# Performance work log

Hardware: AMD Instinct MI355X
Metric: run time of the kernel (lower is better)

Reference implementation:

```python
import jax, jax.numpy as jnp
import numpy as np

TAU = 2.0        # LIFNode tau
ALPHA = 4.0      # spikingjelly default Sigmoid surrogate alpha
SCALE = 0.125    # attention scale from SSA
EPS = 1e-5       # BatchNorm eps

@jax.custom_vjp
def heaviside(x):
    return (x >= 0).astype(x.dtype)

def _hv_fwd(x):
    return (x >= 0).astype(x.dtype), x

def _hv_bwd(x, g):
    s = jax.nn.sigmoid(ALPHA * x)
    return (g * ALPHA * s * (1.0 - s),)

heaviside.defvjp(_hv_fwd, _hv_bwd)

def lif(x_seq, v_th):
    """Multi-step LIF (decay_input=True, v_reset=0, hard reset, detach_reset=True).
    x_seq: (T, ...) -> spikes (T, ...)."""
    def step(v, x):
        h = v + (x - v) / TAU                      # membrane charge
        s = heaviside(h - v_th)                    # spike
        v_new = h * (1.0 - jax.lax.stop_gradient(s))  # detached hard reset to 0
        return v_new, s
    _, spikes = jax.lax.scan(step, jnp.zeros_like(x_seq[0]), x_seq)
    return spikes

def conv_bn(x, w, gamma, beta, mean, var):
    """3x3 same-pad conv (no bias) + BatchNorm2d (eval: running stats), applied over merged T*B."""
    T, B, C, H, W = x.shape
    y = jax.lax.conv_general_dilated(
        x.reshape(T * B, C, H, W), w, (1, 1), 'SAME',
        dimension_numbers=('NCHW', 'OIHW', 'NCHW'))
    scale = gamma / jnp.sqrt(var + EPS)
    y = y * scale[:, None, None] + (beta - mean * scale)[:, None, None]
    return y.reshape(T, B, C, H, W)

def setup_inputs() -> dict:
    key = jax.random.key(0)
    T, B, C, H, W = 4, 16, 768, 16, 16
    ks = jax.random.split(key, 5)
    d = {"x": jax.random.normal(ks[0], (T, B, C, H, W), jnp.float32)}
    for i, p in enumerate(["q", "k", "v", "p"]):
        kk = jax.random.split(ks[i + 1], 5)
        d[p + "_w"] = jax.random.normal(kk[0], (C, C, 3, 3), jnp.float32) * 0.02
        d[p + "_gamma"] = jax.random.uniform(kk[1], (C,), jnp.float32, 0.5, 1.5)
        d[p + "_beta"] = jax.random.normal(kk[2], (C,), jnp.float32) * 0.1
        d[p + "_mean"] = jax.random.normal(kk[3], (C,), jnp.float32) * 0.1
        d[p + "_var"] = jax.random.uniform(kk[4], (C,), jnp.float32, 0.5, 1.5)
    return d

def reference(x, q_w, q_gamma, q_beta, q_mean, q_var,
              k_w, k_gamma, k_beta, k_mean, k_var,
              v_w, v_gamma, v_beta, v_mean, v_var,
              p_w, p_gamma, p_beta, p_mean, p_var):
    T, B, C, H, W = x.shape
    N = H * W
    nh = 8
    dh = C // nh
    xs = lif(x, 1.0)                                   # head_lif
    # Scaler is identity in eval mode (and rate=1.0)
    q = lif(conv_bn(xs, q_w, q_gamma, q_beta, q_mean, q_var), 1.0)
    k = lif(conv_bn(xs, k_w, k_gamma, k_beta, k_mean, k_var), 1.0)
    v = lif(conv_bn(xs, v_w, v_gamma, v_beta, v_mean, v_var), 1.0)
    def to_heads(t):  # (T,B,C,H,W) -> (T,B,nh,N,dh)
        return t.reshape(T, B, C, N).transpose(0, 1, 3, 2).reshape(T, B, N, nh, dh).transpose(0, 1, 3, 2, 4)
    q, k, v = to_heads(q), to_heads(k), to_heads(v)
    kv = jnp.einsum('tbhnd,tbhne->tbhde', k, v)        # k^T @ v (linear attention)
    o = jnp.einsum('tbhnd,tbhde->tbhne', q, kv) * SCALE
    o = o.transpose(0, 1, 2, 4, 3).reshape(T, B, C, N)  # (T,B,h,d,N) -> (T,B,C,N)
    o = lif(o, 0.5).reshape(T, B, C, H, W)              # attn_lif with v_threshold=0.5
    return conv_bn(o, p_w, p_gamma, p_beta, p_mean, p_var)
```

## Files before the change

### kernel.cpp

```cpp
#include <hip/hip_runtime.h>

typedef __attribute__((ext_vector_type(4))) int   i32x4;
typedef __attribute__((ext_vector_type(4))) float f32x4;
typedef unsigned int u32;
typedef unsigned long long u64;
typedef unsigned char u8;
typedef unsigned short u16;

#define C_ 768
#define NPIX 256
#define PLANE (16*C_*NPIX)
#define ROWB 96
#define ROWL 112
#define IMGBITS (324*ROWB)
#define AEXP_STRIDE 80
#define AEXP_SZ 14400

#define OFF_WFRAG 0ull
#define OFF_YBUF  10616832ull
#define OFF_QU8   60948480ull
#define OFF_KU8   73531392ull
#define OFF_VU8   86114304ull
#define OFF_OU8   98697216ull
#define OFF_BITS  111280128ull
#define BITSZ     1990656ull
#define OFF_SBT   121233408ull
#define OFF_FLAGS 121257984ull
#define OFF_WMAX  121258240ull

__device__ __forceinline__ i32x4 as_i4(uint4 v){ union{uint4 u; i32x4 s;} c; c.u=v; return c.s; }
#define SPREAD(NIB) ((u32)__mul24((int)(NIB), 0x204081) & 0x01010101u)

__global__ __launch_bounds__(256) void bn_prep(
    const float* __restrict__ g, const float* __restrict__ be,
    const float* __restrict__ m, const float* __restrict__ va,
    float* __restrict__ out)
{
    int i = blockIdx.x*256 + threadIdx.x;
    if (i < C_){
        float s = g[i] / sqrtf(va[i] + 1e-5f);
        out[i] = s;
        out[C_+i] = be[i] - m[i]*s;
    }
}

__global__ __launch_bounds__(256) void wmax_k(
    const float* __restrict__ w, int n, float* __restrict__ out)
{
    float m = 0.f;
    for (int i = blockIdx.x*256 + threadIdx.x; i < n; i += 131072)
        m = fmaxf(m, fabsf(w[i]));
    #pragma unroll
    for (int off = 32; off >= 1; off >>= 1)
        m = fmaxf(m, __shfl_xor(m, off));
    if ((threadIdx.x & 63) == 0)
        atomicMax((int*)out, __float_as_int(m));
}

__global__ __launch_bounds__(256) void wprep(
    const float* __restrict__ w, const float* __restrict__ wmaxp,
    u8* __restrict__ wf)
{
    int gid = blockIdx.x*256 + threadIdx.x;
    int co = gid / 48, c16 = gid - co*48;
    float mw = *wmaxp;
    float invS = (mw > 0.f) ? (32512.0f / mw) : 0.f;
    int cch = c16 >> 2;
    int lane = (co & 15) | ((c16 & 3) << 4);
    int nfg = co >> 4;
    const float* wp = w + (size_t)co*6912 + (size_t)c16*144;
    #pragma unroll 1
    for (int tap=0; tap<9; ++tap){
        u32 hw[4] = {0,0,0,0}, lw[4] = {0,0,0,0};
        #pragma unroll
        for (int e=0;e<16;++e){
            float f = wp[e*9 + tap];
            int w16 = __float2int_rn(f * invS);
            w16 = min(max(w16, -32512), 32512);
            int hi = (w16 + 128) >> 8;
            int lo = w16 - (hi << 8);
            hw[e>>2] |= ((u32)(hi & 0xFF)) << ((e&3)*8);
            lw[e>>2] |= ((u32)(lo & 0xFF)) << ((e&3)*8);
        }
        size_t base = (((size_t)(cch*9+tap)*48 + nfg)*2)*1024 + (size_t)lane*16;
        *(uint4*)(wf + base)        = make_uint4(hw[0],hw[1],hw[2],hw[3]);
        *(uint4*)(wf + base + 1024) = make_uint4(lw[0],lw[1],lw[2],lw[3]);
    }
}

__global__ __launch_bounds__(256) void head_bits(
    const float* __restrict__ x, u8* __restrict__ bits)
{
    int gid = blockIdx.x*256 + threadIdx.x;
    int b = gid / 24576, rem = gid - b*24576;
    int cb = rem >> 8, pix = rem & 255;
    int pr = ((pix>>4)+1)*18 + (pix&15) + 1;
    float v[8];
    #pragma unroll
    for (int j=0;j<8;++j) v[j]=0.f;
    #pragma unroll
    for (int t=0;t<4;++t){
        int img = t*16 + b;
        u32 byte = 0;
        #pragma unroll
        for (int j=0;j<8;++j){
            float xv = x[((size_t)img*C_ + cb*8 + j)*NPIX + pix];
            float h = __fadd_rn(v[j], __fmul_rn(__fsub_rn(xv, v[j]), 0.5f));
            u32 s = (h >= 1.0f) ? 1u : 0u;
            v[j] = s ? 0.f : h;
            byte |= s << j;
        }
        bits[(size_t)img*IMGBITS + (size_t)pr*ROWB + cb] = (u8)byte;
    }
}

template<int EPI>
__global__ __launch_bounds__(256,2) void conv_i8(
    const u8* __restrict__ abits, const u8* __restrict__ wf,
    const float* __restrict__ sb, const float* __restrict__ wmaxp,
    const int* __restrict__ flags,
    float* __restrict__ ybuf, float* __restrict__ out)
{
    __shared__ __align__(16) u8 Ab[324*ROWL];
    __shared__ __align__(16) u8 Aexp[2*AEXP_SZ];
    const int tid = threadIdx.x;
    const int bid = blockIdx.x;
    const int cox = bid & 7, mh = (bid >> 3) & 1, img = bid >> 4;
    const int lane = tid & 63, w = tid >> 6;
    const int wr = w >> 1, wc = w & 1;
    const int lrow = lane & 15, lgrp = lane >> 4;

    if constexpr (EPI == 1){
        if (flags[img] == 0){
            #pragma unroll 1
            for (int i = tid; i < 96*32; i += 256){
                int co = cox*96 + (i >> 5), seg = i & 31;
                float bv = sb[C_ + co];
                f32x4 v; v[0]=bv; v[1]=bv; v[2]=bv; v[3]=bv;
                *(f32x4*)(out + ((size_t)img*C_ + co)*NPIX + mh*128 + seg*4) = v;
            }
            return;
        }
    }

    {
        const u8* src = abits + (size_t)img*IMGBITS;
        #pragma unroll 1
        for (int r = tid; r < 324; r += 256){
            const u8* s = src + r*ROWB;
            u8* d = Ab + r*ROWL;
            #pragma unroll
            for (int j=0;j<6;++j) *(uint4*)(d + j*16) = *(const uint4*)(s + j*16);
        }
    }

    const u8* wp = wf + (size_t)((cox*6 + wc*3)*2)*1024 + (size_t)lane*16;
    uint4 B0[6], B1[6];
#define LOADB(BUF) { \
    _Pragma("unroll") \
    for (int j=0;j<6;++j) BUF[j] = *(const uint4*)(wp + (j>>1)*2048 + (j&1)*1024); \
    wp += 98304; }

    LOADB(B0);
    __syncthreads();

#define EXPAND(CCH, BUFOFF) if (tid < 180){ \
    const u8* sp = Ab + (mh*144 + tid)*ROWL + (CCH)*8; \
    u32 blo = *(const u32*)(sp); u32 bhi = *(const u32*)(sp + 4); \
    u8* dp = Aexp + (BUFOFF) + tid*AEXP_STRIDE; \
    *(uint4*)(dp)    = make_uint4(SPREAD(blo&0xF), SPREAD((blo>>4)&0xF), SPREAD((blo>>8)&0xF), SPREAD((blo>>12)&0xF)); \
    *(uint4*)(dp+16) = make_uint4(SPREAD((blo>>16)&0xF), SPREAD((blo>>20)&0xF), SPREAD((blo>>24)&0xF), SPREAD((blo>>28)&0xF)); \
    *(uint4*)(dp+32) = make_uint4(SPREAD(bhi&0xF), SPREAD((bhi>>4)&0xF), SPREAD((bhi>>8)&0xF), SPREAD((bhi>>12)&0xF)); \
    *(uint4*)(dp+48) = make_uint4(SPREAD((bhi>>16)&0xF), SPREAD((bhi>>20)&0xF), SPREAD((bhi>>24)&0xF), SPREAD((bhi>>28)&0xF)); }

    EXPAND(0, 0);
    __syncthreads();

    int rb[4];
    #pragma unroll
    for (int mi=0;mi<4;++mi)
        rb[mi] = (wr*4 + mi + 1)*1440 + (lrow + 1)*AEXP_STRIDE + lgrp*16;

    i32x4 acc_h[4][3], acc_l[4][3];
    #pragma unroll
    for (int mi=0;mi<4;++mi)
        #pragma unroll
        for (int ni=0;ni<3;++ni)
            #pragma unroll
            for (int r=0;r<4;++r){ acc_h[mi][ni][r]=0; acc_l[mi][ni][r]=0; }

#define COMPUTE(BUF, AE, TAP) { \
    const int DT = ((TAP)/3 - 1)*1440 + (((TAP)%3) - 1)*AEXP_STRIDE; \
    i32x4 af[4]; \
    _Pragma("unroll") \
    for (int mi=0;mi<4;++mi) af[mi] = *(const i32x4*)((AE) + rb[mi] + DT); \
    __builtin_amdgcn_s_setprio(1); \
    _Pragma("unroll") \
    for (int mi=0;mi<4;++mi){ \
        _Pragma("unroll") \
        for (int ni=0;ni<3;++ni){ \
            acc_h[mi][ni] = __builtin_amdgcn_mfma_i32_16x16x64_i8(af[mi], as_i4(BUF[ni*2+0]), acc_h[mi][ni], 0,0,0); \
            acc_l[mi][ni] = __builtin_amdgcn_mfma_i32_16x16x64_i8(af[mi], as_i4(BUF[ni*2+1]), acc_l[mi][ni], 0,0,0); \
        } \
    } \
    __builtin_amdgcn_s_setprio(0); }

#define CCH_BODY(X, Y, CCH, BUFOFF, DO_EXP) { \
    if (DO_EXP) EXPAND((CCH)+1, (BUFOFF) ^ AEXP_SZ); \
    const u8* Ae = Aexp + (BUFOFF); \
    _Pragma("unroll") \
    for (int tp=0; tp<8; tp+=2){ \
        LOADB(Y); COMPUTE(X, Ae, tp); \
        LOADB(X); COMPUTE(Y, Ae, tp+1); \
    } \
    LOADB(Y); COMPUTE(X, Ae, 8); \
    __syncthreads(); }

    #pragma unroll 1
    for (int c2=0; c2<6; ++c2){
        CCH_BODY(B0, B1, 2*c2,     0,       true);
        CCH_BODY(B1, B0, 2*c2+1,   AEXP_SZ, (c2 < 5));
    }
#undef LOADB
#undef EXPAND
#undef COMPUTE
#undef CCH_BODY

    const float S = (*wmaxp) * (1.0f/32512.0f);
    #pragma unroll
    for (int mi=0;mi<4;++mi){
        const int prow = mh*128 + wr*64 + mi*16 + lgrp*4;
        #pragma unroll
        for (int ni=0;ni<3;++ni){
            const int co = cox*96 + wc*48 + ni*16 + lrow;
            const float sc = sb[co], bi = sb[C_ + co];
            if constexpr (EPI == 0){
                #pragma unroll
                for (int r=0;r<4;++r){
                    float accf = (float)(acc_h[mi][ni][r]*256 + acc_l[mi][ni][r]) * S;
                    ybuf[((size_t)img*NPIX + prow + r)*C_ + co] =
                        __fadd_rn(__fmul_rn(accf, sc), bi);
                }
            } else {
                f32x4 ov;
                #pragma unroll
                for (int r=0;r<4;++r){
                    float accf = (float)(acc_h[mi][ni][r]*256 + acc_l[mi][ni][r]) * S;
                    ov[r] = __fadd_rn(__fmul_rn(accf, sc), bi);
                }
                *(f32x4*)(out + ((size_t)img*C_ + co)*NPIX + prow) = ov;
            }
        }
    }
}

__global__ __launch_bounds__(256) void lif_bits(
    const float* __restrict__ y, u8* __restrict__ su8, u8* __restrict__ bits)
{
    int gid = blockIdx.x*256 + threadIdx.x;
    int b = gid / 24576, rem = gid - b*24576;
    int pix = rem / 96, cb = rem - pix*96;
    int pr = ((pix>>4)+1)*18 + (pix&15) + 1;
    float v[8];
    #pragma unroll
    for (int j=0;j<8;++j) v[j]=0.f;
    #pragma unroll
    for (int t=0;t<4;++t){
        int img = t*16 + b;
        const float* yp = y + ((size_t)img*NPIX + pix)*C_ + cb*8;
        f32x4 y0 = *(const f32x4*)yp;
        f32x4 y1 = *(const f32x4*)(yp + 4);
        u32 byte = 0, w0 = 0, w1 = 0;
        #pragma unroll
        for (int j=0;j<8;++j){
            float yv = (j<4) ? y0[j] : y1[j-4];
            float h = __fadd_rn(v[j], __fmul_rn(__fsub_rn(yv, v[j]), 0.5f));
            u32 s = (h >= 1.0f) ? 1u : 0u;
            v[j] = s ? 0.f : h;
            byte |= s << j;
            if (j<4) w0 |= s << (j*8); else w1 |= s << ((j-4)*8);
        }
        *(uint2*)(su8 + ((size_t)img*NPIX + pix)*C_ + cb*8) = make_uint2(w0,w1);
        bits[(size_t)img*IMGBITS + (size_t)pr*ROWB + cb] = (u8)byte;
    }
}

__global__ __launch_bounds__(256) void pad_o_bits(
    const u8* __restrict__ o, u8* __restrict__ bits, int* __restrict__ flags)
{
    int gid = blockIdx.x*256 + threadIdx.x;
    int img = gid / 24576, rem = gid - img*24576;
    int pix = rem / 96, cb = rem - pix*96;
    int pr = ((pix>>4)+1)*18 + (pix&15) + 1;
    uint2 r = *(const uint2*)(o + ((size_t)img*NPIX + pix)*C_ + cb*8);
    u32 byte = 0;
    #pragma unroll
    for (int j=0;j<4;++j){
        byte |= ((r.x >> (j*8)) & 1u) << j;
        byte |= ((r.y >> (j*8)) & 1u) << (j+4);
    }
    bits[(size_t)img*IMGBITS + (size_t)pr*ROWB + cb] = (u8)byte;
    if (__any((int)(r.x | r.y)) && (threadIdx.x & 63) == 0)
        atomicOr(&flags[img], 1);
}

__global__ __launch_bounds__(512) void attn_fused(
    const u8* __restrict__ qs, const u8* __restrict__ ks,
    const u8* __restrict__ vs, u8* __restrict__ os)
{
    const int tid = threadIdx.x;
    const int b = blockIdx.x, h = blockIdx.y;
    __shared__ u64 kb[96][4], vb[96][4];
    __shared__ float kvl[96][96];
    const int w = tid >> 6, lane = tid & 63;
    const int ng = w & 3, n_build = ng*64 + lane;
    const int n = tid & 255, eh = tid >> 8;
    float vmem[48];
    #pragma unroll
    for (int e=0;e<48;++e) vmem[e]=0.f;

    for (int t=0;t<4;++t){
        const int img = t*16 + b;
        const size_t rbase = ((size_t)img*NPIX)*C_ + (size_t)h*96;
        {
            const u8* src = (w < 4 ? ks : vs) + rbase + (size_t)n_build*C_;
            uint4 r[6];
            #pragma unroll
            for (int j=0;j<6;++j) r[j] = ((const uint4*)src)[j];
            u32 wd[24];
            #pragma unroll
            for (int j=0;j<6;++j){ wd[4*j]=r[j].x; wd[4*j+1]=r[j].y; wd[4*j+2]=r[j].z; wd[4*j+3]=r[j].w; }
            u64 (*dst)[4] = (w < 4) ? kb : vb;
            #pragma unroll 1
            for (int d=0; d<96; ++d){
                u32 byte = (wd[d>>2] >> ((d&3)*8)) & 0xFFu;
                u64 m = __ballot((int)byte);
                if (lane == 0) dst[d][ng] = m;
            }
        }
        __syncthreads();
        for (int i = tid; i < 96*96; i += 512){
            int d = i / 96, e = i - d*96;
            int s = 0;
            #pragma unroll
            for (int g=0; g<4; ++g) s += __popcll(kb[d][g] & vb[e][g]);
            kvl[d][e] = (float)s;
        }
        __syncthreads();
        {
            const u8* qsrc = qs + rbase + (size_t)n*C_;
            uint4 r[6];
            #pragma unroll
            for (int j=0;j<6;++j) r[j] = ((const uint4*)qsrc)[j];
            u32 qw[24];
            #pragma unroll
            for (int j=0;j<6;++j){ qw[4*j]=r[j].x; qw[4*j+1]=r[j].y; qw[4*j+2]=r[j].z; qw[4*j+3]=r[j].w; }
            float val[48];
            #pragma unroll
            for (int e=0;e<48;++e) val[e]=0.f;
            #pragma unroll 1
            for (int d=0; d<96; ++d){
                u32 qb = (qw[d>>2] >> ((d&3)*8)) & 0xFFu;
                if (__any((int)qb)){
                    float qf = (float)qb;
                    #pragma unroll
                    for (int e=0;e<48;++e) val[e] += qf * kvl[d][eh*48+e];
                }
            }
            u32 ow[12];
            #pragma unroll
            for (int e=0;e<48;++e){
                float o = val[e]*0.125f;
                float hh = __fadd_rn(vmem[e], __fmul_rn(__fsub_rn(o, vmem[e]), 0.5f));
                u8 s = (hh >= 0.5f) ? 1 : 0;
                vmem[e] = s ? 0.f : hh;
                if ((e&3)==0) ow[e>>2] = (u32)s; else ow[e>>2] |= ((u32)s) << ((e&3)*8);
            }
            uint4* od = (uint4*)(os + rbase + (size_t)n*C_ + eh*48);
            od[0] = make_uint4(ow[0],ow[1],ow[2],ow[3]);
            od[1] = make_uint4(ow[4],ow[5],ow[6],ow[7]);
            od[2] = make_uint4(ow[8],ow[9],ow[10],ow[11]);
        }
        __syncthreads();
    }
}

extern "C" void kernel_launch(void* const* d_in, const int* in_sizes, int n_in,
                              void* d_out, int out_size, void* d_ws, size_t ws_size,
                              hipStream_t stream)
{
    u8* ws = (u8*)d_ws;
    u8* wfrag   = ws + OFF_WFRAG;
    float* ybuf = (float*)(ws + OFF_YBUF);
    u8* q_u8 = ws + OFF_QU8;
    u8* k_u8 = ws + OFF_KU8;
    u8* v_u8 = ws + OFF_VU8;
    u8* o_u8 = ws + OFF_OU8;
    u8* xs_b = ws + OFF_BITS;
    u8* q_b  = ws + OFF_BITS + 1*BITSZ;
    u8* k_b  = ws + OFF_BITS + 2*BITSZ;
    u8* v_b  = ws + OFF_BITS + 3*BITSZ;
    u8* o_b  = ws + OFF_BITS + 4*BITSZ;
    float* sbt = (float*)(ws + OFF_SBT);
    int* flags = (int*)(ws + OFF_FLAGS);
    float* wmaxb = (float*)(ws + OFF_WMAX);
    float* outp = (float*)d_out;
    const int WN = 9*C_*C_;

    hipMemsetAsync(ws + OFF_BITS, 0, 5*BITSZ, stream);
    hipMemsetAsync(ws + OFF_FLAGS, 0, 512, stream);

    for (int s=0;s<4;++s)
        bn_prep<<<3,256,0,stream>>>((const float*)d_in[2+5*s], (const float*)d_in[3+5*s],
                                    (const float*)d_in[4+5*s], (const float*)d_in[5+5*s],
                                    sbt + s*1536);
    head_bits<<<1536,256,0,stream>>>((const float*)d_in[0], xs_b);

    u8* u8p[3]  = {q_u8, k_u8, v_u8};
    u8* bitp[3] = {q_b, k_b, v_b};
    for (int s=0;s<3;++s){
        wmax_k<<<512,256,0,stream>>>((const float*)d_in[1+5*s], WN, wmaxb + s);
        wprep<<<144,256,0,stream>>>((const float*)d_in[1+5*s], wmaxb + s, wfrag);
        conv_i8<0><<<1024,256,0,stream>>>(xs_b, wfrag, sbt + s*1536, wmaxb + s,
                                          nullptr, ybuf, nullptr);
        lif_bits<<<1536,256,0,stream>>>(ybuf, u8p[s], bitp[s]);
    }
    attn_fused<<<dim3(16,8),512,0,stream>>>(q_u8, k_u8, v_u8, o_u8);
    pad_o_bits<<<6144,256,0,stream>>>(o_u8, o_b, flags);
    wmax_k<<<512,256,0,stream>>>((const float*)d_in[16], WN, wmaxb + 3);
    wprep<<<144,256,0,stream>>>((const float*)d_in[16], wmaxb + 3, wfrag);
    conv_i8<1><<<1024,256,0,stream>>>(o_b, wfrag, sbt + 4608, wmaxb + 3,
                                      flags, nullptr, outp);
}
```

Baseline: 683.2 us.

## Stream activation bits from global in conv, triple-buffer weights, batch prep kernels

The conv kernel no longer stages the whole bit-packed image tile in LDS. Each channel chunk's bits are loaded directly from global into a register, prefetched one chunk ahead, and expanded into a double-buffered LDS area with a new layout that splits 16-channel groups by pixel. This cuts LDS use, which may raise occupancy, and drops one staging pass and one barrier. Weight fragment prefetch goes from two to three register buffers, at the cost of more register pressure. Separately, the four BN-prep launches and four weight-max launches are each merged into one batched launch, and the weight-max kernel now reads float4 vectors.

```diff
diff --git a/kernel.cpp b/kernel.cpp
--- a/kernel.cpp
+++ b/kernel.cpp
@@ -11,10 +11,10 @@
 #define NPIX 256
 #define PLANE (16*C_*NPIX)
 #define ROWB 96
-#define ROWL 112
 #define IMGBITS (324*ROWB)
-#define AEXP_STRIDE 80
-#define AEXP_SZ 14400
+#define GS   304
+#define PRS  1232
+#define AEXP_SZ 12320
 
 #define OFF_WFRAG 0ull
 #define OFF_YBUF  10616832ull
@@ -31,30 +31,49 @@
 __device__ __forceinline__ i32x4 as_i4(uint4 v){ union{uint4 u; i32x4 s;} c; c.u=v; return c.s; }
 #define SPREAD(NIB) ((u32)__mul24((int)(NIB), 0x204081) & 0x01010101u)
 
-__global__ __launch_bounds__(256) void bn_prep(
-    const float* __restrict__ g, const float* __restrict__ be,
-    const float* __restrict__ m, const float* __restrict__ va,
+__global__ __launch_bounds__(256) void bn_prep4(
+    const float* __restrict__ g0, const float* __restrict__ b0,
+    const float* __restrict__ m0, const float* __restrict__ v0,
+    const float* __restrict__ g1, const float* __restrict__ b1,
+    const float* __restrict__ m1, const float* __restrict__ v1,
+    const float* __restrict__ g2, const float* __restrict__ b2,
+    const float* __restrict__ m2, const float* __restrict__ v2,
+    const float* __restrict__ g3, const float* __restrict__ b3,
+    const float* __restrict__ m3, const float* __restrict__ v3,
     float* __restrict__ out)
 {
+    int s = blockIdx.y;
+    const float* g  = s==0?g0:s==1?g1:s==2?g2:g3;
+    const float* be = s==0?b0:s==1?b1:s==2?b2:b3;
+    const float* m  = s==0?m0:s==1?m1:s==2?m2:m3;
+    const float* va = s==0?v0:s==1?v1:s==2?v2:v3;
     int i = blockIdx.x*256 + threadIdx.x;
     if (i < C_){
-        float s = g[i] / sqrtf(va[i] + 1e-5f);
-        out[i] = s;
-        out[C_+i] = be[i] - m[i]*s;
-    }
-}
-
-__global__ __launch_bounds__(256) void wmax_k(
-    const float* __restrict__ w, int n, float* __restrict__ out)
-{
+        float sc = g[i] / sqrtf(va[i] + 1e-5f);
+        out[s*1536 + i] = sc;
+        out[s*1536 + C_ + i] = be[i] - m[i]*sc;
+    }
+}
+
+__global__ __launch_bounds__(256) void wmax4(
+    const float* __restrict__ w0, const float* __restrict__ w1,
+    const float* __restrict__ w2, const float* __restrict__ w3,
+    float* __restrict__ out)
+{
+    int s = blockIdx.y;
+    const float* w = s==0?w0:s==1?w1:s==2?w2:w3;
+    const int n4 = 9*C_*C_/4;
     float m = 0.f;
-    for (int i = blockIdx.x*256 + threadIdx.x; i < n; i += 131072)
-        m = fmaxf(m, fabsf(w[i]));
+    for (int i = blockIdx.x*256 + threadIdx.x; i < n4; i += 65536){
+        f32x4 v = *(const f32x4*)(w + (size_t)i*4);
+        m = fmaxf(m, fmaxf(fmaxf(fabsf(v[0]), fabsf(v[1])),
+                           fmaxf(fabsf(v[2]), fabsf(v[3]))));
+    }
     #pragma unroll
     for (int off = 32; off >= 1; off >>= 1)
         m = fmaxf(m, __shfl_xor(m, off));
     if ((threadIdx.x & 63) == 0)
-        atomicMax((int*)out, __float_as_int(m));
+        atomicMax((int*)(out + s), __float_as_int(m));
 }
 
 __global__ __launch_bounds__(256) void wprep(
@@ -121,7 +140,6 @@
     const int* __restrict__ flags,
     float* __restrict__ ybuf, float* __restrict__ out)
 {
-    __shared__ __align__(16) u8 Ab[324*ROWL];
     __shared__ __align__(16) u8 Aexp[2*AEXP_SZ];
     const int tid = threadIdx.x;
     const int bid = blockIdx.x;
@@ -143,43 +161,30 @@
         }
     }
 
-    {
-        const u8* src = abits + (size_t)img*IMGBITS;
-        #pragma unroll 1
-        for (int r = tid; r < 324; r += 256){
-            const u8* s = src + r*ROWB;
-            u8* d = Ab + r*ROWL;
-            #pragma unroll
-            for (int j=0;j<6;++j) *(uint4*)(d + j*16) = *(const uint4*)(s + j*16);
-        }
-    }
+    const int erow = (tid < 180) ? tid : 179;
+    const int epr = erow / 18, epc = erow - epr*18;
+    u8* edst = Aexp + epr*PRS + epc*16;
+    const u8* bsrc = abits + (size_t)img*IMGBITS + (size_t)(mh*144)*ROWB;
+
+#define EXPW(BW, BOFF) if (tid < 180){ \
+    u8* dp = edst + (BOFF); \
+    u32 lo_ = (u32)(BW), hi_ = (u32)((BW)>>32); \
+    *(uint4*)(dp       ) = make_uint4(SPREAD(lo_&0xF), SPREAD((lo_>>4)&0xF), SPREAD((lo_>>8)&0xF), SPREAD((lo_>>12)&0xF)); \
+    *(uint4*)(dp + GS  ) = make_uint4(SPREAD((lo_>>16)&0xF), SPREAD((lo_>>20)&0xF), SPREAD((lo_>>24)&0xF), SPREAD((lo_>>28)&0xF)); \
+    *(uint4*)(dp + 2*GS) = make_uint4(SPREAD(hi_&0xF), SPREAD((hi_>>4)&0xF), SPREAD((hi_>>8)&0xF), SPREAD((hi_>>12)&0xF)); \
+    *(uint4*)(dp + 3*GS) = make_uint4(SPREAD((hi_>>16)&0xF), SPREAD((hi_>>20)&0xF), SPREAD((hi_>>24)&0xF), SPREAD((hi_>>28)&0xF)); }
 
     const u8* wp = wf + (size_t)((cox*6 + wc*3)*2)*1024 + (size_t)lane*16;
-    uint4 B0[6], B1[6];
+    uint4 R0[6], R1[6], R2[6];
 #define LOADB(BUF) { \
     _Pragma("unroll") \
     for (int j=0;j<6;++j) BUF[j] = *(const uint4*)(wp + (j>>1)*2048 + (j&1)*1024); \
     wp += 98304; }
 
-    LOADB(B0);
-    __syncthreads();
-
-#define EXPAND(CCH, BUFOFF) if (tid < 180){ \
-    const u8* sp = Ab + (mh*144 + tid)*ROWL + (CCH)*8; \
-    u32 blo = *(const u32*)(sp); u32 bhi = *(const u32*)(sp + 4); \
-    u8* dp = Aexp + (BUFOFF) + tid*AEXP_STRIDE; \
-    *(uint4*)(dp)    = make_uint4(SPREAD(blo&0xF), SPREAD((blo>>4)&0xF), SPREAD((blo>>8)&0xF), SPREAD((blo>>12)&0xF)); \
-    *(uint4*)(dp+16) = make_uint4(SPREAD((blo>>16)&0xF), SPREAD((blo>>20)&0xF), SPREAD((blo>>24)&0xF), SPREAD((blo>>28)&0xF)); \
-    *(uint4*)(dp+32) = make_uint4(SPREAD(bhi&0xF), SPREAD((bhi>>4)&0xF), SPREAD((bhi>>8)&0xF), SPREAD((bhi>>12)&0xF)); \
-    *(uint4*)(dp+48) = make_uint4(SPREAD((bhi>>16)&0xF), SPREAD((bhi>>20)&0xF), SPREAD((bhi>>24)&0xF), SPREAD((bhi>>28)&0xF)); }
-
-    EXPAND(0, 0);
-    __syncthreads();
-
     int rb[4];
     #pragma unroll
     for (int mi=0;mi<4;++mi)
-        rb[mi] = (wr*4 + mi + 1)*1440 + (lrow + 1)*AEXP_STRIDE + lgrp*16;
+        rb[mi] = (wr*4 + mi + 1)*PRS + lgrp*GS + (lrow+1)*16;
 
     i32x4 acc_h[4][3], acc_l[4][3];
     #pragma unroll
@@ -190,7 +195,7 @@
             for (int r=0;r<4;++r){ acc_h[mi][ni][r]=0; acc_l[mi][ni][r]=0; }
 
 #define COMPUTE(BUF, AE, TAP) { \
-    const int DT = ((TAP)/3 - 1)*1440 + (((TAP)%3) - 1)*AEXP_STRIDE; \
+    const int DT = ((TAP)/3 - 1)*PRS + (((TAP)%3) - 1)*16; \
     i32x4 af[4]; \
     _Pragma("unroll") \
     for (int mi=0;mi<4;++mi) af[mi] = *(const i32x4*)((AE) + rb[mi] + DT); \
@@ -205,26 +210,38 @@
     } \
     __builtin_amdgcn_s_setprio(0); }
 
-#define CCH_BODY(X, Y, CCH, BUFOFF, DO_EXP) { \
-    if (DO_EXP) EXPAND((CCH)+1, (BUFOFF) ^ AEXP_SZ); \
-    const u8* Ae = Aexp + (BUFOFF); \
-    _Pragma("unroll") \
-    for (int tp=0; tp<8; tp+=2){ \
-        LOADB(Y); COMPUTE(X, Ae, tp); \
-        LOADB(X); COMPUTE(Y, Ae, tp+1); \
-    } \
-    LOADB(Y); COMPUTE(X, Ae, 8); \
+#define BODY(CCH, BOFF) { \
+    u64 bwn = 0; \
+    if ((CCH) < 11) bwn = *(const u64*)(bsrc + erow*ROWB + ((CCH)+1)*8); \
+    const u8* Ae = Aexp + (BOFF); \
+    LOADB(R2); COMPUTE(R0, Ae, 0); \
+    LOADB(R0); COMPUTE(R1, Ae, 1); \
+    LOADB(R1); COMPUTE(R2, Ae, 2); \
+    LOADB(R2); COMPUTE(R0, Ae, 3); \
+    LOADB(R0); COMPUTE(R1, Ae, 4); \
+    LOADB(R1); COMPUTE(R2, Ae, 5); \
+    LOADB(R2); COMPUTE(R0, Ae, 6); \
+    LOADB(R0); COMPUTE(R1, Ae, 7); \
+    LOADB(R1); COMPUTE(R2, Ae, 8); \
+    if ((CCH) < 11) EXPW(bwn, (BOFF) ^ AEXP_SZ); \
     __syncthreads(); }
+
+    LOADB(R0); LOADB(R1);
+    {
+        u64 bw0 = *(const u64*)(bsrc + erow*ROWB);
+        EXPW(bw0, 0);
+    }
+    __syncthreads();
 
     #pragma unroll 1
     for (int c2=0; c2<6; ++c2){
-        CCH_BODY(B0, B1, 2*c2,     0,       true);
-        CCH_BODY(B1, B0, 2*c2+1,   AEXP_SZ, (c2 < 5));
+        BODY(2*c2,   0);
+        BODY(2*c2+1, AEXP_SZ);
     }
 #undef LOADB
-#undef EXPAND
+#undef EXPW
 #undef COMPUTE
-#undef CCH_BODY
+#undef BODY
 
     const float S = (*wmaxp) * (1.0f/32512.0f);
     #pragma unroll
@@ -405,21 +422,24 @@
     int* flags = (int*)(ws + OFF_FLAGS);
     float* wmaxb = (float*)(ws + OFF_WMAX);
     float* outp = (float*)d_out;
-    const int WN = 9*C_*C_;
 
     hipMemsetAsync(ws + OFF_BITS, 0, 5*BITSZ, stream);
     hipMemsetAsync(ws + OFF_FLAGS, 0, 512, stream);
 
-    for (int s=0;s<4;++s)
-        bn_prep<<<3,256,0,stream>>>((const float*)d_in[2+5*s], (const float*)d_in[3+5*s],
-                                    (const float*)d_in[4+5*s], (const float*)d_in[5+5*s],
-                                    sbt + s*1536);
+    bn_prep4<<<dim3(3,4),256,0,stream>>>(
+        (const float*)d_in[2],  (const float*)d_in[3],  (const float*)d_in[4],  (const float*)d_in[5],
+        (const float*)d_in[7],  (const float*)d_in[8],  (const float*)d_in[9],  (const float*)d_in[10],
+        (const float*)d_in[12], (const float*)d_in[13], (const float*)d_in[14], (const float*)d_in[15],
+        (const float*)d_in[17], (const float*)d_in[18], (const float*)d_in[19], (const float*)d_in[20],
+        sbt);
+    wmax4<<<dim3(256,4),256,0,stream>>>(
+        (const float*)d_in[1], (const float*)d_in[6],
+        (const float*)d_in[11], (const float*)d_in[16], wmaxb);
     head_bits<<<1536,256,0,stream>>>((const float*)d_in[0], xs_b);
 
     u8* u8p[3]  = {q_u8, k_u8, v_u8};
     u8* bitp[3] = {q_b, k_b, v_b};
     for (int s=0;s<3;++s){
-        wmax_k<<<512,256,0,stream>>>((const float*)d_in[1+5*s], WN, wmaxb + s);
         wprep<<<144,256,0,stream>>>((const float*)d_in[1+5*s], wmaxb + s, wfrag);
         conv_i8<0><<<1024,256,0,stream>>>(xs_b, wfrag, sbt + s*1536, wmaxb + s,
                                           nullptr, ybuf, nullptr);
@@ -427,7 +447,6 @@
     }
     attn_fused<<<dim3(16,8),512,0,stream>>>(q_u8, k_u8, v_u8, o_u8);
     pad_o_bits<<<6144,256,0,stream>>>(o_u8, o_b, flags);
-    wmax_k<<<512,256,0,stream>>>((const float*)d_in[16], WN, wmaxb + 3);
     wprep<<<144,256,0,stream>>>((const float*)d_in[16], wmaxb + 3, wfrag);
     conv_i8<1><<<1024,256,0,stream>>>(o_b, wfrag, sbt + 4608, wmaxb + 3,
                                       flags, nullptr, outp);
```

Result: faster. 600.7 us (-12.1%).
